# Kernel optimization log

Measured on AMD Instinct MI355X. Metric: run time of the kernel, lower is better.

## Reference

```python
import jax, jax.numpy as jnp
import numpy as np

HIDDEN = 1024
HEADS = 16
HEAD_DIM = HIDDEN // HEADS
BATCH = 2
SEQ = 2048
ROPE_BASE = 10000.0


def rotate_half(x):
    x1, x2 = x[..., : x.shape[-1] // 2], x[..., x.shape[-1] // 2 :]
    return jnp.concatenate((-x2, x1), axis=-1)


def rope_cos_sin(seq_len, dim, dtype=jnp.float32):
    inv_freq = 1.0 / (ROPE_BASE ** (jnp.arange(0, dim, 2, dtype=jnp.float32) / dim))
    t = jnp.arange(seq_len, dtype=jnp.float32)
    freqs = jnp.einsum('i,j->ij', t, inv_freq)          # [S, dim/2]
    emb = jnp.concatenate((freqs, freqs), axis=-1)       # [S, dim]
    return emb.astype(dtype).cos(), emb.astype(dtype).sin() if False else (jnp.cos(emb).astype(dtype), jnp.sin(emb).astype(dtype))[0], None


def _rope(seq_len, dim):
    inv_freq = 1.0 / (ROPE_BASE ** (jnp.arange(0, dim, 2, dtype=jnp.float32) / dim))
    t = jnp.arange(seq_len, dtype=jnp.float32)
    freqs = jnp.einsum('i,j->ij', t, inv_freq)
    emb = jnp.concatenate((freqs, freqs), axis=-1)
    return jnp.cos(emb), jnp.sin(emb)  # each [S, dim]


def setup_inputs() -> dict:
    key = jax.random.key(0)
    ks = jax.random.split(key, 9)
    scale = 1.0 / np.sqrt(HIDDEN)
    inp = {
        'hidden_states': jax.random.normal(ks[0], (BATCH, SEQ, HIDDEN), dtype=jnp.float32),
        'Wq': jax.random.uniform(ks[1], (HIDDEN, HIDDEN), minval=-scale, maxval=scale, dtype=jnp.float32),
        'bq': jax.random.uniform(ks[2], (HIDDEN,), minval=-scale, maxval=scale, dtype=jnp.float32),
        'Wk': jax.random.uniform(ks[3], (HIDDEN, HIDDEN), minval=-scale, maxval=scale, dtype=jnp.float32),
        'bk': jax.random.uniform(ks[4], (HIDDEN,), minval=-scale, maxval=scale, dtype=jnp.float32),
        'Wv': jax.random.uniform(ks[5], (HIDDEN, HIDDEN), minval=-scale, maxval=scale, dtype=jnp.float32),
        'bv': jax.random.uniform(ks[6], (HIDDEN,), minval=-scale, maxval=scale, dtype=jnp.float32),
        'Wo': jax.random.uniform(ks[7], (HIDDEN, HIDDEN), minval=-scale, maxval=scale, dtype=jnp.float32),
        'bo': jax.random.uniform(ks[8], (HIDDEN,), minval=-scale, maxval=scale, dtype=jnp.float32),
    }
    return inp


def reference(hidden_states, Wq, bq, Wk, bk, Wv, bv, Wo, bo):
    B, S, H = hidden_states.shape
    # projections (torch Linear: x @ W.T + b), split into heads: [B, nH, S, hd]
    def proj(W, b):
        y = hidden_states @ W.T + b
        return y.reshape(B, S, HEADS, HEAD_DIM).transpose(0, 2, 1, 3)

    q = proj(Wq, bq)
    k = proj(Wk, bk)
    v = proj(Wv, bv)

    cos, sin = _rope(S, HEAD_DIM)  # [S, hd], broadcast over B, nH
    q = q * cos + rotate_half(q) * sin
    k = k * cos + rotate_half(k) * sin

    scale = 1.0 / jnp.sqrt(jnp.array(HEAD_DIM, dtype=q.dtype))
    logits = jnp.einsum('bhqd,bhkd->bhqk', q, k) * scale  # [B, nH, S, S]
    attn = jax.nn.softmax(logits, axis=-1)
    out = jnp.einsum('bhqk,bhkd->bhqd', attn, v)           # [B, nH, S, hd]
    out = out.transpose(0, 2, 1, 3).reshape(B, S, H)
    return out @ Wo.T + bo
```

## Files before the change

kernel.cpp:

```cpp
#include <hip/hip_runtime.h>
#include <hip/hip_bf16.h>
#include <math.h>

#define HIDDEN 1024
#define NH 16
#define HD 64
#define BATCH 2
#define SEQ 2048

typedef __attribute__((ext_vector_type(8))) short bf16x8;
typedef __attribute__((ext_vector_type(4))) float f32x4;

static __device__ __forceinline__ unsigned short f2b(float f) {
    __hip_bfloat16 h = __float2bfloat16(f);
    return __builtin_bit_cast(unsigned short, h);
}

static __device__ __forceinline__ float fexp2(float x) {
    return __builtin_amdgcn_exp2f(x);
}

static __device__ __forceinline__ void async16(const unsigned short* g, unsigned short* l) {
    __builtin_amdgcn_global_load_lds(
        (const __attribute__((address_space(1))) unsigned int*)g,
        (__attribute__((address_space(3))) unsigned int*)l, 16, 0, 0);
}

__global__ __launch_bounds__(256)
void cvt_bf16(const float* __restrict__ X,
              const float* __restrict__ Wq, const float* __restrict__ Wk,
              const float* __restrict__ Wv, const float* __restrict__ Wo,
              unsigned short* __restrict__ dst)
{
    const size_t g = (size_t)blockIdx.x * 256 + threadIdx.x;
    const float* src;
    size_t local;
    if (g < 1048576) {
        src = X; local = g;
    } else {
        const size_t gg = g - 1048576;
        const int r = (int)(gg >> 18);
        local = gg & 262143;
        src = (r == 0) ? Wq : ((r == 1) ? Wk : ((r == 2) ? Wv : Wo));
    }
    const float4 v = *(const float4*)(src + local * 4);
    ushort4 o;
    o.x = f2b(v.x); o.y = f2b(v.y); o.z = f2b(v.z); o.w = f2b(v.w);
    *(ushort4*)(dst + g * 4) = o;
}

__global__ __launch_bounds__(256, 2)
void qkv_rope(const unsigned short* __restrict__ X,
              const unsigned short* __restrict__ Wqb, const float* __restrict__ bq,
              const unsigned short* __restrict__ Wkb, const float* __restrict__ bk,
              const unsigned short* __restrict__ Wvb, const float* __restrict__ bv,
              unsigned short* __restrict__ qw, unsigned short* __restrict__ kw,
              unsigned short* __restrict__ vw)
{
    const int proj = blockIdx.y >> 3;
    const unsigned short* W = (proj == 0) ? Wqb : ((proj == 1) ? Wkb : Wvb);
    const float* bias       = (proj == 0) ? bq : ((proj == 1) ? bk : bv);
    unsigned short* outp    = (proj == 0) ? qw : ((proj == 1) ? kw : vw);
    const int tn = (blockIdx.y & 7) * 128;
    const int tm = blockIdx.x * 128;

    __shared__ __align__(16) unsigned short As[128 * 32];
    __shared__ __align__(16) unsigned short Bs[128 * 32];

    const int tid  = threadIdx.x;
    const int lane = tid & 63;
    const int wave = tid >> 6;
    const int quad = lane >> 4;
    const int l16  = lane & 15;
    const int wm   = (wave & 1) * 64;
    const int wn   = (wave >> 1) * 64;

    const int r0 = tid >> 2;
    const int c0 = (tid & 3) * 8;
    const unsigned short* Ag = X + (size_t)(tm + r0) * HIDDEN + c0;
    const unsigned short* Bg = W + (size_t)(tn + r0) * HIDDEN + c0;
    unsigned short* lA = As + tid * 8;
    unsigned short* lB = Bs + tid * 8;

    f32x4 acc[4][4] = {};

    for (int k0 = 0; k0 < HIDDEN; k0 += 32) {
        __syncthreads();
        async16(Ag + k0, lA);
        async16(Ag + 64 * HIDDEN + k0, lA + 2048);
        async16(Bg + k0, lB);
        async16(Bg + 64 * HIDDEN + k0, lB + 2048);
        __syncthreads();
        bf16x8 af[4], bfr[4];
#pragma unroll
        for (int i = 0; i < 4; ++i)
            af[i] = *(const bf16x8*)(As + (wm + i * 16 + l16) * 32 + quad * 8);
#pragma unroll
        for (int j = 0; j < 4; ++j)
            bfr[j] = *(const bf16x8*)(Bs + (wn + j * 16 + l16) * 32 + quad * 8);
#pragma unroll
        for (int i = 0; i < 4; ++i)
#pragma unroll
            for (int j = 0; j < 4; ++j)
                acc[i][j] = __builtin_amdgcn_mfma_f32_16x16x32_bf16(af[i], bfr[j], acc[i][j], 0, 0, 0);
    }

    const bool dorope = (proj < 2);
    float bsv[4];
#pragma unroll
    for (int j = 0; j < 4; ++j) bsv[j] = bias[tn + wn + j * 16 + l16];
    float inv_e = 0.f, inv_o = 0.f;
    if (dorope) {
        const float LB = 0.4152410118609203f;
        inv_e = exp2f(-LB * (float)l16);
        inv_o = exp2f(-LB * (float)(16 + l16));
    }
#pragma unroll
    for (int i = 0; i < 4; ++i) {
#pragma unroll
        for (int r = 0; r < 4; ++r) {
            const int m = tm + wm + i * 16 + quad * 4 + r;
            const int b = m >> 11;
            const int s = m & (SEQ - 1);
            float cs0 = 1.f, sn0 = 0.f, cs1 = 1.f, sn1 = 0.f;
            if (dorope) {
                const float sf = (float)s;
                __sincosf(sf * inv_e, &sn0, &cs0);
                __sincosf(sf * inv_o, &sn1, &cs1);
            }
#pragma unroll
            for (int j = 0; j < 4; ++j) {
                const int n = tn + wn + j * 16 + l16;
                const float v = acc[i][j][r] + bsv[j];
                float o = v;
                if (dorope) {
                    const float vp = acc[i][j ^ 2][r] + bsv[j ^ 2];
                    o = v * ((j & 1) ? cs1 : cs0) + ((j < 2) ? -vp : vp) * ((j & 1) ? sn1 : sn0);
                }
                const int h = n >> 6;
                const int d = n & 63;
                outp[(((size_t)(b * NH + h)) * SEQ + s) * HD + d] = f2b(o);
            }
        }
    }
}

__global__ __launch_bounds__(256, 2)
void attn_fwd(const unsigned short* __restrict__ qb, const unsigned short* __restrict__ kb,
              const unsigned short* __restrict__ vb, unsigned short* __restrict__ ob)
{
    const int flat  = blockIdx.y * gridDim.x + blockIdx.x;
    const int flat2 = (flat & 7) * 64 + (flat >> 3);
    const int bh = flat2 >> 4;
    const int qt = flat2 & 15;
    const int b  = bh >> 4;
    const int h  = bh & 15;
    const unsigned short* Q = qb + (size_t)bh * SEQ * HD;
    const unsigned short* K = kb + (size_t)bh * SEQ * HD;
    const unsigned short* V = vb + (size_t)bh * SEQ * HD;

    const int tid  = threadIdx.x;
    const int wave = tid >> 6;
    const int lane = tid & 63;
    const int quad = lane >> 4;
    const int l16  = lane & 15;
    const int q0   = qt * 128 + wave * 32;

    __shared__ __align__(16) unsigned short Pb[4][32 * 136];
    __shared__ __align__(16) unsigned short Vt[64 * 136];

    bf16x8 qf[2][2];
#pragma unroll
    for (int mt = 0; mt < 2; ++mt)
#pragma unroll
        for (int kk = 0; kk < 2; ++kk)
            qf[mt][kk] = *(const bf16x8*)(Q + (size_t)(q0 + mt * 16 + l16) * HD + kk * 32 + quad * 8);

    f32x4 oacc[2][4] = {};
    float mr[2][4], lr[2][4];
#pragma unroll
    for (int mt = 0; mt < 2; ++mt)
#pragma unroll
        for (int r = 0; r < 4; ++r) { mr[mt][r] = -3.0e38f; lr[mt][r] = 0.f; }

    const int vkey = tid >> 3;
    const int vd0  = (tid & 7) * 8;
    const int vm   = tid & 7;

    const float KSCL = 0.18033688011112042f;

    for (int kt = 0; kt < SEQ / 128; ++kt) {
        const int t0 = kt * 128;

        f32x4 sc[2][8] = {};
#pragma unroll
        for (int kk = 0; kk < 2; ++kk) {
            bf16x8 kf[8];
#pragma unroll
            for (int jj = 0; jj < 8; ++jj)
                kf[jj] = *(const bf16x8*)(K + (size_t)(t0 + jj * 16 + l16) * HD + kk * 32 + quad * 8);
#pragma unroll
            for (int mt = 0; mt < 2; ++mt)
#pragma unroll
                for (int jj = 0; jj < 8; ++jj)
                    sc[mt][jj] = __builtin_amdgcn_mfma_f32_16x16x32_bf16(qf[mt][kk], kf[jj], sc[mt][jj], 0, 0, 0);
        }

        __syncthreads();

#pragma unroll
        for (int p = 0; p < 4; ++p) {
            const int ky = vkey + 32 * p;
            const int cs = ky ^ (vm << 3);
            bf16x8 vv = *(const bf16x8*)(V + (size_t)(t0 + ky) * HD + vd0);
#pragma unroll
            for (int u = 0; u < 8; ++u)
                Vt[(vd0 + u) * 136 + cs] = ((const unsigned short*)&vv)[u];
        }

        float dmax = -3.0e38f;
#pragma unroll
        for (int mt = 0; mt < 2; ++mt) {
#pragma unroll
            for (int r = 0; r < 4; ++r) {
                float mx = sc[mt][0][r];
#pragma unroll
                for (int jj = 1; jj < 8; ++jj) mx = fmaxf(mx, sc[mt][jj][r]);
                dmax = fmaxf(dmax, fmaf(mx, KSCL, -mr[mt][r]));
            }
        }
        if (!__all(dmax <= 8.0f)) {
#pragma unroll
            for (int mt = 0; mt < 2; ++mt) {
#pragma unroll
                for (int r = 0; r < 4; ++r) {
                    float mx = sc[mt][0][r];
#pragma unroll
                    for (int jj = 1; jj < 8; ++jj) mx = fmaxf(mx, sc[mt][jj][r]);
                    float ms = mx * KSCL;
#pragma unroll
                    for (int off = 8; off; off >>= 1) ms = fmaxf(ms, __shfl_xor(ms, off));
                    const float mnew  = fmaxf(mr[mt][r], ms);
                    const float alpha = fexp2(mr[mt][r] - mnew);
                    mr[mt][r] = mnew;
                    lr[mt][r] *= alpha;
#pragma unroll
                    for (int nn = 0; nn < 4; ++nn) oacc[mt][nn][r] *= alpha;
                }
            }
        }
#pragma unroll
        for (int mt = 0; mt < 2; ++mt) {
#pragma unroll
            for (int r = 0; r < 4; ++r) {
                const float mnew = mr[mt][r];
                float ps = 0.f;
                const int prow = (mt * 16 + quad * 4 + r) * 136;
#pragma unroll
                for (int jj = 0; jj < 8; ++jj) {
                    const float p = fexp2(fmaf(sc[mt][jj][r], KSCL, -mnew));
                    ps += p;
                    Pb[wave][prow + jj * 16 + l16] = f2b(p);
                }
                lr[mt][r] += ps;
            }
        }

        __syncthreads();

#pragma unroll
        for (int kk2 = 0; kk2 < 4; ++kk2) {
            bf16x8 pf[2], vf[4];
#pragma unroll
            for (int mt = 0; mt < 2; ++mt)
                pf[mt] = *(const bf16x8*)(&Pb[wave][(mt * 16 + l16) * 136 + kk2 * 32 + quad * 8]);
#pragma unroll
            for (int nn = 0; nn < 4; ++nn) {
                const int d   = nn * 16 + l16;
                const int mrd = (nn * 2 + (l16 >> 3)) & 7;
                const int cb  = (kk2 * 32 + quad * 8) ^ (mrd << 3);
                vf[nn] = *(const bf16x8*)(&Vt[d * 136 + cb]);
            }
#pragma unroll
            for (int mt = 0; mt < 2; ++mt)
#pragma unroll
                for (int nn = 0; nn < 4; ++nn)
                    oacc[mt][nn] = __builtin_amdgcn_mfma_f32_16x16x32_bf16(pf[mt], vf[nn], oacc[mt][nn], 0, 0, 0);
        }
    }

#pragma unroll
    for (int mt = 0; mt < 2; ++mt) {
#pragma unroll
        for (int r = 0; r < 4; ++r) {
            float ls = lr[mt][r];
#pragma unroll
            for (int off = 8; off; off >>= 1) ls += __shfl_xor(ls, off);
            const float inv = 1.0f / ls;
            const int s = q0 + mt * 16 + quad * 4 + r;
#pragma unroll
            for (int nn = 0; nn < 4; ++nn) {
                const int d = nn * 16 + l16;
                ob[((size_t)(b * SEQ + s)) * HIDDEN + h * HD + d] = f2b(oacc[mt][nn][r] * inv);
            }
        }
    }
}

__global__ __launch_bounds__(256, 2)
void out_proj(const unsigned short* __restrict__ A,
              const unsigned short* __restrict__ W,
              const float* __restrict__ bias,
              float* __restrict__ out)
{
    const int tn = blockIdx.y * 64;
    const int tm = blockIdx.x * 128;

    __shared__ __align__(16) unsigned short As[128 * 32];
    __shared__ __align__(16) unsigned short Bs[64 * 32];

    const int tid  = threadIdx.x;
    const int lane = tid & 63;
    const int wave = tid >> 6;
    const int quad = lane >> 4;
    const int l16  = lane & 15;
    const int wm   = (wave & 1) * 64;
    const int wn   = (wave >> 1) * 32;

    const int r0 = tid >> 2;
    const int c0 = (tid & 3) * 8;
    const unsigned short* Ag = A + (size_t)(tm + r0) * HIDDEN + c0;
    const unsigned short* Bg = W + (size_t)(tn + r0) * HIDDEN + c0;
    unsigned short* lA = As + tid * 8;
    unsigned short* lB = Bs + tid * 8;

    f32x4 acc[4][2] = {};

    for (int k0 = 0; k0 < HIDDEN; k0 += 32) {
        __syncthreads();
        async16(Ag + k0, lA);
        async16(Ag + 64 * HIDDEN + k0, lA + 2048);
        async16(Bg + k0, lB);
        __syncthreads();
        bf16x8 af[4], bfr[2];
#pragma unroll
        for (int i = 0; i < 4; ++i)
            af[i] = *(const bf16x8*)(As + (wm + i * 16 + l16) * 32 + quad * 8);
#pragma unroll
        for (int j = 0; j < 2; ++j)
            bfr[j] = *(const bf16x8*)(Bs + (wn + j * 16 + l16) * 32 + quad * 8);
#pragma unroll
        for (int i = 0; i < 4; ++i)
#pragma unroll
            for (int j = 0; j < 2; ++j)
                acc[i][j] = __builtin_amdgcn_mfma_f32_16x16x32_bf16(af[i], bfr[j], acc[i][j], 0, 0, 0);
    }

    float bsv[2];
#pragma unroll
    for (int j = 0; j < 2; ++j) bsv[j] = bias[tn + wn + j * 16 + l16];
#pragma unroll
    for (int i = 0; i < 4; ++i) {
#pragma unroll
        for (int r = 0; r < 4; ++r) {
            const int m = tm + wm + i * 16 + quad * 4 + r;
#pragma unroll
            for (int j = 0; j < 2; ++j) {
                const int n = tn + wn + j * 16 + l16;
                out[(size_t)m * HIDDEN + n] = acc[i][j][r] + bsv[j];
            }
        }
    }
}

extern "C" void kernel_launch(void* const* d_in, const int* in_sizes, int n_in,
                              void* d_out, int out_size, void* d_ws, size_t ws_size,
                              hipStream_t stream) {
    const float* hs = (const float*)d_in[0];
    const float* Wq = (const float*)d_in[1];
    const float* bq = (const float*)d_in[2];
    const float* Wk = (const float*)d_in[3];
    const float* bk = (const float*)d_in[4];
    const float* Wv = (const float*)d_in[5];
    const float* bv = (const float*)d_in[6];
    const float* Wo = (const float*)d_in[7];
    const float* bo = (const float*)d_in[8];
    float* out = (float*)d_out;

    unsigned short* Xb  = (unsigned short*)d_ws;
    unsigned short* Wqb = Xb + 4194304;
    unsigned short* Wkb = Wqb + 1048576;
    unsigned short* Wvb = Wkb + 1048576;
    unsigned short* Wob = Wvb + 1048576;
    unsigned short* qw  = Wob + 1048576;
    unsigned short* kw  = qw + 4194304;
    unsigned short* vw  = kw + 4194304;
    unsigned short* aw  = vw + 4194304;

    cvt_bf16<<<dim3(8192), 256, 0, stream>>>(hs, Wq, Wk, Wv, Wo, Xb);
    qkv_rope<<<dim3(32, 24), 256, 0, stream>>>(Xb, Wqb, bq, Wkb, bk, Wvb, bv, qw, kw, vw);
    attn_fwd<<<dim3(16, 32), 256, 0, stream>>>(qw, kw, vw, aw);
    out_proj<<<dim3(32, 16), 256, 0, stream>>>(aw, Wob, bo, out);
}
```

Before: 226.1 us.

## Double K-tile depth to 64 with XOR-swizzled LDS layout in projection GEMMs

Both projection GEMMs (QKV+RoPE and output) now load 64-wide K slices per iteration instead of 32. This halves the number of barrier pairs and gives more MFMA work per sync. The global-to-LDS source columns are XOR-swizzled by row so the 128-byte LDS rows can be read without bank conflicts. The QKV kernel's launch bound also asks for 3 blocks per CU, which costs more LDS per block and caps registers more tightly.

```diff
diff --git a/kernel.cpp b/kernel.cpp
--- a/kernel.cpp
+++ b/kernel.cpp
@@ -49,7 +49,7 @@
     *(ushort4*)(dst + g * 4) = o;
 }
 
-__global__ __launch_bounds__(256, 2)
+__global__ __launch_bounds__(256, 3)
 void qkv_rope(const unsigned short* __restrict__ X,
               const unsigned short* __restrict__ Wqb, const float* __restrict__ bq,
               const unsigned short* __restrict__ Wkb, const float* __restrict__ bk,
@@ -64,8 +64,8 @@
     const int tn = (blockIdx.y & 7) * 128;
     const int tm = blockIdx.x * 128;
 
-    __shared__ __align__(16) unsigned short As[128 * 32];
-    __shared__ __align__(16) unsigned short Bs[128 * 32];
+    __shared__ __align__(16) unsigned short As[128 * 64];
+    __shared__ __align__(16) unsigned short Bs[128 * 64];
 
     const int tid  = threadIdx.x;
     const int lane = tid & 63;
@@ -75,34 +75,42 @@
     const int wm   = (wave & 1) * 64;
     const int wn   = (wave >> 1) * 64;
 
-    const int r0 = tid >> 2;
-    const int c0 = (tid & 3) * 8;
-    const unsigned short* Ag = X + (size_t)(tm + r0) * HIDDEN + c0;
-    const unsigned short* Bg = W + (size_t)(tn + r0) * HIDDEN + c0;
+    const int srow = tid >> 3;
+    const int sccx = (tid & 7) ^ (srow & 7);
+    const unsigned short* Ag = X + (size_t)(tm + srow) * HIDDEN + sccx * 8;
+    const unsigned short* Bg = W + (size_t)(tn + srow) * HIDDEN + sccx * 8;
     unsigned short* lA = As + tid * 8;
     unsigned short* lB = Bs + tid * 8;
 
     f32x4 acc[4][4] = {};
 
-    for (int k0 = 0; k0 < HIDDEN; k0 += 32) {
-        __syncthreads();
-        async16(Ag + k0, lA);
-        async16(Ag + 64 * HIDDEN + k0, lA + 2048);
-        async16(Bg + k0, lB);
-        async16(Bg + 64 * HIDDEN + k0, lB + 2048);
-        __syncthreads();
-        bf16x8 af[4], bfr[4];
-#pragma unroll
-        for (int i = 0; i < 4; ++i)
-            af[i] = *(const bf16x8*)(As + (wm + i * 16 + l16) * 32 + quad * 8);
-#pragma unroll
-        for (int j = 0; j < 4; ++j)
-            bfr[j] = *(const bf16x8*)(Bs + (wn + j * 16 + l16) * 32 + quad * 8);
-#pragma unroll
-        for (int i = 0; i < 4; ++i)
-#pragma unroll
-            for (int j = 0; j < 4; ++j)
-                acc[i][j] = __builtin_amdgcn_mfma_f32_16x16x32_bf16(af[i], bfr[j], acc[i][j], 0, 0, 0);
+    for (int k0 = 0; k0 < HIDDEN; k0 += 64) {
+        __syncthreads();
+#pragma unroll
+        for (int p = 0; p < 4; ++p) {
+            async16(Ag + k0 + p * 32 * HIDDEN, lA + p * 2048);
+            async16(Bg + k0 + p * 32 * HIDDEN, lB + p * 2048);
+        }
+        __syncthreads();
+#pragma unroll
+        for (int c = 0; c < 2; ++c) {
+            bf16x8 af[4], bfr[4];
+#pragma unroll
+            for (int i = 0; i < 4; ++i) {
+                const int row = wm + i * 16 + l16;
+                af[i] = *(const bf16x8*)(As + row * 64 + (((c * 4 + quad) ^ (l16 & 7)) * 8));
+            }
+#pragma unroll
+            for (int j = 0; j < 4; ++j) {
+                const int row = wn + j * 16 + l16;
+                bfr[j] = *(const bf16x8*)(Bs + row * 64 + (((c * 4 + quad) ^ (l16 & 7)) * 8));
+            }
+#pragma unroll
+            for (int i = 0; i < 4; ++i)
+#pragma unroll
+                for (int j = 0; j < 4; ++j)
+                    acc[i][j] = __builtin_amdgcn_mfma_f32_16x16x32_bf16(af[i], bfr[j], acc[i][j], 0, 0, 0);
+        }
     }
 
     const bool dorope = (proj < 2);
@@ -316,8 +324,8 @@
     const int tn = blockIdx.y * 64;
     const int tm = blockIdx.x * 128;
 
-    __shared__ __align__(16) unsigned short As[128 * 32];
-    __shared__ __align__(16) unsigned short Bs[64 * 32];
+    __shared__ __align__(16) unsigned short As[128 * 64];
+    __shared__ __align__(16) unsigned short Bs[64 * 64];
 
     const int tid  = threadIdx.x;
     const int lane = tid & 63;
@@ -327,33 +335,43 @@
     const int wm   = (wave & 1) * 64;
     const int wn   = (wave >> 1) * 32;
 
-    const int r0 = tid >> 2;
-    const int c0 = (tid & 3) * 8;
-    const unsigned short* Ag = A + (size_t)(tm + r0) * HIDDEN + c0;
-    const unsigned short* Bg = W + (size_t)(tn + r0) * HIDDEN + c0;
+    const int srow = tid >> 3;
+    const int sccx = (tid & 7) ^ (srow & 7);
+    const unsigned short* Ag = A + (size_t)(tm + srow) * HIDDEN + sccx * 8;
+    const unsigned short* Bg = W + (size_t)(tn + srow) * HIDDEN + sccx * 8;
     unsigned short* lA = As + tid * 8;
     unsigned short* lB = Bs + tid * 8;
 
     f32x4 acc[4][2] = {};
 
-    for (int k0 = 0; k0 < HIDDEN; k0 += 32) {
-        __syncthreads();
-        async16(Ag + k0, lA);
-        async16(Ag + 64 * HIDDEN + k0, lA + 2048);
-        async16(Bg + k0, lB);
-        __syncthreads();
-        bf16x8 af[4], bfr[2];
-#pragma unroll
-        for (int i = 0; i < 4; ++i)
-            af[i] = *(const bf16x8*)(As + (wm + i * 16 + l16) * 32 + quad * 8);
-#pragma unroll
-        for (int j = 0; j < 2; ++j)
-            bfr[j] = *(const bf16x8*)(Bs + (wn + j * 16 + l16) * 32 + quad * 8);
-#pragma unroll
-        for (int i = 0; i < 4; ++i)
-#pragma unroll
-            for (int j = 0; j < 2; ++j)
-                acc[i][j] = __builtin_amdgcn_mfma_f32_16x16x32_bf16(af[i], bfr[j], acc[i][j], 0, 0, 0);
+    for (int k0 = 0; k0 < HIDDEN; k0 += 64) {
+        __syncthreads();
+#pragma unroll
+        for (int p = 0; p < 4; ++p)
+            async16(Ag + k0 + p * 32 * HIDDEN, lA + p * 2048);
+#pragma unroll
+        for (int p = 0; p < 2; ++p)
+            async16(Bg + k0 + p * 32 * HIDDEN, lB + p * 2048);
+        __syncthreads();
+#pragma unroll
+        for (int c = 0; c < 2; ++c) {
+            bf16x8 af[4], bfr[2];
+#pragma unroll
+            for (int i = 0; i < 4; ++i) {
+                const int row = wm + i * 16 + l16;
+                af[i] = *(const bf16x8*)(As + row * 64 + (((c * 4 + quad) ^ (l16 & 7)) * 8));
+            }
+#pragma unroll
+            for (int j = 0; j < 2; ++j) {
+                const int row = wn + j * 16 + l16;
+                bfr[j] = *(const bf16x8*)(Bs + row * 64 + (((c * 4 + quad) ^ (l16 & 7)) * 8));
+            }
+#pragma unroll
+            for (int i = 0; i < 4; ++i)
+#pragma unroll
+                for (int j = 0; j < 2; ++j)
+                    acc[i][j] = __builtin_amdgcn_mfma_f32_16x16x32_bf16(af[i], bfr[j], acc[i][j], 0, 0, 0);
+        }
     }
 
     float bsv[2];
```

New measurement: 219.5 us. 2.9% less time.
